# Optimization experiments

Measured on AMD Instinct MI355X. Metric: run time of the kernel, lower is better.

## Reference

```python
import jax, jax.numpy as jnp
import numpy as np

N_NODES = 50000   # total nodes across the batch of graphs
N_EDGES = 800000  # avg degree 16
F_IN = 128        # num_features
DIM = 256         # hidden dim
N_LAYERS = 3      # num_gc_layers
N_GRAPHS = 512    # graphs in the batch (max(batch)+1)
BN_EPS = 1e-5


def setup_inputs() -> dict:
    key = jax.random.key(0)
    ks = jax.random.split(key, 16)
    inp = {}
    inp["x"] = jax.random.normal(ks[0], (N_NODES, F_IN), dtype=jnp.float32)
    inp["edge_index"] = jax.random.randint(ks[1], (2, N_EDGES), 0, N_NODES, dtype=jnp.int64)
    inp["batch"] = jnp.sort(jax.random.randint(ks[2], (N_NODES,), 0, N_GRAPHS, dtype=jnp.int64))
    k = 3
    for i in range(N_LAYERS):
        fin = F_IN if i == 0 else DIM
        inp[f"w1_{i}"] = jax.random.normal(ks[k], (fin, DIM), dtype=jnp.float32) / np.sqrt(fin); k += 1
        inp[f"b1_{i}"] = jnp.zeros((DIM,), dtype=jnp.float32)
        inp[f"w2_{i}"] = jax.random.normal(ks[k], (DIM, DIM), dtype=jnp.float32) / np.sqrt(DIM); k += 1
        inp[f"b2_{i}"] = jnp.zeros((DIM,), dtype=jnp.float32)
        inp[f"bn_g{i}"] = jnp.ones((DIM,), dtype=jnp.float32)
        inp[f"bn_b{i}"] = jnp.zeros((DIM,), dtype=jnp.float32)
    return inp


def _gin_layer(h, src, dst, w1, b1, w2, b2, g, b):
    # GINConv (eps=0): agg_i = h_i + sum_{j->i} h_j  (scatter-add over edges)
    agg = h + jax.ops.segment_sum(h[src], dst, num_segments=N_NODES)
    # MLP: Linear -> ReLU -> Linear
    m = jnp.maximum(agg @ w1 + b1, 0.0) @ w2 + b2
    # F.relu then BatchNorm1d (training mode: batch statistics, biased var)
    m = jnp.maximum(m, 0.0)
    mu = m.mean(axis=0)
    var = ((m - mu) ** 2).mean(axis=0)
    return g * (m - mu) / jnp.sqrt(var + BN_EPS) + b


def reference(x, edge_index, batch,
              w1_0, b1_0, w2_0, b2_0, bn_g0, bn_b0,
              w1_1, b1_1, w2_1, b2_1, bn_g1, bn_b1,
              w1_2, b1_2, w2_2, b2_2, bn_g2, bn_b2):
    src, dst = edge_index[0], edge_index[1]
    params = [
        (w1_0, b1_0, w2_0, b2_0, bn_g0, bn_b0),
        (w1_1, b1_1, w2_1, b2_1, bn_g1, bn_b1),
        (w1_2, b1_2, w2_2, b2_2, bn_g2, bn_b2),
    ]
    xs = []
    h = x
    for p in params:
        h = _gin_layer(h, src, dst, *p)
        xs.append(h)
    # global add-pool readout per layer, concat along feature dim
    pooled = jnp.concatenate(
        [jax.ops.segment_sum(hi, batch, num_segments=N_GRAPHS) for hi in xs], axis=1)
    return pooled, jnp.concatenate(xs, axis=1)
```

## Files before the change

kernel.cpp:

```cpp
#include <hip/hip_runtime.h>

#define N_NODES 50000
#define N_EDGES 800000
#define F_IN 128
#define DIM 256
#define N_GRAPHS 512
#define BN_EPS 1e-5f

typedef unsigned short u16;
typedef unsigned int u32;
using floatx4 = __attribute__((ext_vector_type(4))) float;
using short8 = __attribute__((ext_vector_type(8))) short;

__device__ __forceinline__ u16 f2b(float f) {
    u32 u = __float_as_uint(f);
    return (u16)((u + 0x7fffu + ((u >> 16) & 1u)) >> 16);
}
__device__ __forceinline__ float blo(u32 u) { return __uint_as_float(u << 16); }
__device__ __forceinline__ float bhi(u32 u) { return __uint_as_float(u & 0xffff0000u); }
__device__ __forceinline__ u32 pack2(float a, float b) {
    return (u32)f2b(a) | ((u32)f2b(b) << 16);
}
__device__ __forceinline__ void load_lds16(const void* g, void* l) {
    __builtin_amdgcn_global_load_lds((const __attribute__((address_space(1))) void*)g,
                                     (__attribute__((address_space(3))) void*)l, 16, 0, 0);
}


__global__ void count_deg(const int* __restrict__ dst, int* __restrict__ deg, int nE) {
    int e = blockIdx.x * 256 + threadIdx.x;
    if (e < nE) atomicAdd(&deg[dst[e]], 1);
}

__global__ void scan_block(const int* __restrict__ deg, int* __restrict__ row_start,
                           int* __restrict__ bsum, int n) {
    __shared__ int wtot[4];
    int i = blockIdx.x * 256 + threadIdx.x;
    int lane = threadIdx.x & 63, w = threadIdx.x >> 6;
    int v = (i < n) ? deg[i] : 0;
    int s = v;
#pragma unroll
    for (int d = 1; d < 64; d <<= 1) {
        int t = __shfl_up(s, d);
        if (lane >= d) s += t;
    }
    if (lane == 63) wtot[w] = s;
    __syncthreads();
    int off = 0;
#pragma unroll
    for (int k = 0; k < 4; ++k)
        if (k < w) off += wtot[k];
    s += off;
    if (i < n) row_start[i + 1] = s;
    if (threadIdx.x == 255) bsum[blockIdx.x] = s;
}

__global__ void scan_partials(const int* __restrict__ bsum, int* __restrict__ boff,
                              int* __restrict__ row_start, int* __restrict__ cursor, int nb) {
    __shared__ int wtot[4];
    int i = threadIdx.x;
    int lane = i & 63, w = i >> 6;
    int v = (i < nb) ? bsum[i] : 0;
    int s = v;
#pragma unroll
    for (int d = 1; d < 64; d <<= 1) {
        int t = __shfl_up(s, d);
        if (lane >= d) s += t;
    }
    if (lane == 63) wtot[w] = s;
    __syncthreads();
    int off = 0;
#pragma unroll
    for (int k = 0; k < 4; ++k)
        if (k < w) off += wtot[k];
    boff[i] = s + off - v;
    if (i == 0) { row_start[0] = 0; cursor[0] = 0; }
}

__global__ void add_offsets(int* __restrict__ row_start, int* __restrict__ cursor,
                            const int* __restrict__ boff, int n) {
    int i = blockIdx.x * 256 + threadIdx.x;
    if (i < n) {
        int fin = row_start[i + 1] + boff[blockIdx.x];
        row_start[i + 1] = fin;
        cursor[i + 1] = fin;
    }
}

__global__ void fill_csr(const int* __restrict__ src, const int* __restrict__ dst,
                         int* __restrict__ cursor, int* __restrict__ srcs, int nE) {
    int e = blockIdx.x * 256 + threadIdx.x;
    if (e < nE) {
        int p = atomicAdd(&cursor[dst[e]], 1);
        srcs[p] = src[e];
    }
}


__global__ void convert_x4(const float4* __restrict__ in, uint2* __restrict__ out, int n4) {
    int i = blockIdx.x * 256 + threadIdx.x;
    if (i < n4) {
        float4 v = in[i];
        uint2 p;
        p.x = pack2(v.x, v.y);
        p.y = pack2(v.z, v.w);
        out[i] = p;
    }
}

__global__ void conv_wt(const float* __restrict__ w, u16* __restrict__ wt, int K) {
    int idx = blockIdx.x * 256 + threadIdx.x;
    if (idx >= 256 * K) return;
    int nn = idx / K, kk = idx - nn * K;
    wt[idx] = f2b(w[(size_t)kk * 256 + nn]);
}


template <int F>
__global__ void aggregate_bf16(const u16* __restrict__ h, const int* __restrict__ row_start,
                               const int* __restrict__ srcs, u16* __restrict__ outp, int n) {
    constexpr int NWD = F / 128;
    int node = (int)(((size_t)blockIdx.x * blockDim.x + threadIdx.x) >> 6);
    int lane = threadIdx.x & 63;
    if (node >= n) return;
    const u32* base = (const u32*)h;
    int cw = lane * NWD;
    float acc[2 * NWD];
#pragma unroll
    for (int t = 0; t < NWD; ++t) {
        u32 v0 = base[(size_t)node * (F / 2) + cw + t];
        acc[2 * t] = blo(v0);
        acc[2 * t + 1] = bhi(v0);
    }
    int s = row_start[node], e = row_start[node + 1];
    for (int j0 = s; j0 < e; j0 += 64) {
        int myidx = (j0 + lane < e) ? srcs[j0 + lane] : 0;
        int cnt = min(64, e - j0);
        int j = 0;
        for (; j + 3 < cnt; j += 4) {
            int s0 = __shfl(myidx, j);
            int s1 = __shfl(myidx, j + 1);
            int s2 = __shfl(myidx, j + 2);
            int s3 = __shfl(myidx, j + 3);
            u32 a0[NWD], a1[NWD], a2[NWD], a3[NWD];
#pragma unroll
            for (int t = 0; t < NWD; ++t) a0[t] = base[(size_t)s0 * (F / 2) + cw + t];
#pragma unroll
            for (int t = 0; t < NWD; ++t) a1[t] = base[(size_t)s1 * (F / 2) + cw + t];
#pragma unroll
            for (int t = 0; t < NWD; ++t) a2[t] = base[(size_t)s2 * (F / 2) + cw + t];
#pragma unroll
            for (int t = 0; t < NWD; ++t) a3[t] = base[(size_t)s3 * (F / 2) + cw + t];
#pragma unroll
            for (int t = 0; t < NWD; ++t) {
                acc[2 * t]     += (blo(a0[t]) + blo(a1[t])) + (blo(a2[t]) + blo(a3[t]));
                acc[2 * t + 1] += (bhi(a0[t]) + bhi(a1[t])) + (bhi(a2[t]) + bhi(a3[t]));
            }
        }
        for (; j < cnt; ++j) {
            int s0 = __shfl(myidx, j);
            u32 a0[NWD];
#pragma unroll
            for (int t = 0; t < NWD; ++t) a0[t] = base[(size_t)s0 * (F / 2) + cw + t];
#pragma unroll
            for (int t = 0; t < NWD; ++t) {
                acc[2 * t] += blo(a0[t]);
                acc[2 * t + 1] += bhi(a0[t]);
            }
        }
    }
    u32* op = (u32*)outp;
#pragma unroll
    for (int t = 0; t < NWD; ++t)
        op[(size_t)node * (F / 2) + cw + t] = pack2(acc[2 * t], acc[2 * t + 1]);
}


template <int MODE>
__global__ __launch_bounds__(256) void gemm_mfma(
    const u16* __restrict__ A, const u16* __restrict__ Bt, const float* __restrict__ bias,
    void* __restrict__ Cout, float* __restrict__ sums, int M, int K) {
    __shared__ u16 As[128 * 32];
    __shared__ u16 Bs[128 * 32];
    const int tid = threadIdx.x;
    const int w = tid >> 6, lane = tid & 63;
    const int wm = w >> 1, wn = w & 1;
    const int r = lane & 15, rg = lane >> 4;
    const int bm = blockIdx.x * 128;
    const int bn = blockIdx.y * 128;

    floatx4 acc[4][4];
#pragma unroll
    for (int i = 0; i < 4; ++i)
#pragma unroll
        for (int j = 0; j < 4; ++j) acc[i][j] = (floatx4){0.f, 0.f, 0.f, 0.f};

    for (int k0 = 0; k0 < K; k0 += 32) {
        __syncthreads();
#pragma unroll
        for (int q = 0; q < 2; ++q) {
            int i = q * 256 + tid;
            int ar = bm + (i >> 2);
            if (ar >= M) ar = M - 1;
            load_lds16(A + (size_t)ar * K + k0 + (i & 3) * 8, As + (q * 4 + w) * 512);
            int nr = bn + (i >> 2);
            load_lds16(Bt + (size_t)nr * K + k0 + (i & 3) * 8, Bs + (q * 4 + w) * 512);
        }
        __syncthreads();
        short8 a[4], b[4];
#pragma unroll
        for (int mi = 0; mi < 4; ++mi)
            a[mi] = *(const short8*)(As + (wm * 64 + mi * 16 + r) * 32 + rg * 8);
#pragma unroll
        for (int ni = 0; ni < 4; ++ni)
            b[ni] = *(const short8*)(Bs + (wn * 64 + ni * 16 + r) * 32 + rg * 8);
#pragma unroll
        for (int mi = 0; mi < 4; ++mi)
#pragma unroll
            for (int ni = 0; ni < 4; ++ni)
                acc[mi][ni] = __builtin_amdgcn_mfma_f32_16x16x32_bf16(a[mi], b[ni], acc[mi][ni], 0, 0, 0);
    }

    if (MODE == 0) {
        u16* C = (u16*)Cout;
#pragma unroll
        for (int ni = 0; ni < 4; ++ni) {
            int col = bn + wn * 64 + ni * 16 + r;
            float bv = bias[col];
#pragma unroll
            for (int mi = 0; mi < 4; ++mi)
#pragma unroll
                for (int rr = 0; rr < 4; ++rr) {
                    int row = bm + wm * 64 + mi * 16 + rg * 4 + rr;
                    if (row < M) C[(size_t)row * 256 + col] = f2b(fmaxf(acc[mi][ni][rr] + bv, 0.f));
                }
        }
    } else {
        float* C = (float*)Cout;
#pragma unroll
        for (int ni = 0; ni < 4; ++ni) {
            int col = bn + wn * 64 + ni * 16 + r;
            float bv = bias[col];
            float s = 0.f, s2 = 0.f;
#pragma unroll
            for (int mi = 0; mi < 4; ++mi)
#pragma unroll
                for (int rr = 0; rr < 4; ++rr) {
                    int row = bm + wm * 64 + mi * 16 + rg * 4 + rr;
                    if (row < M) {
                        float v = fmaxf(acc[mi][ni][rr] + bv, 0.f);
                        C[(size_t)row * 256 + col] = v;
                        s += v;
                        s2 += v * v;
                    }
                }
            s += __shfl_xor(s, 16);
            s += __shfl_xor(s, 32);
            s2 += __shfl_xor(s2, 16);
            s2 += __shfl_xor(s2, 32);
            if (rg == 0) {
                atomicAdd(&sums[col], s);
                atomicAdd(&sums[256 + col], s2);
            }
        }
    }
}


__global__ void bn_finalize(const float* __restrict__ sums, const float* __restrict__ g,
                            const float* __restrict__ b, float* __restrict__ ss, float inv_n) {
    int c = threadIdx.x;
    float mu = sums[c] * inv_n;
    float var = sums[256 + c] * inv_n - mu * mu;
    float sc = g[c] / sqrtf(var + BN_EPS);
    ss[c] = sc;
    ss[256 + c] = b[c] - mu * sc;
}


template <int WRITE_H>
__global__ void bn_apply_pool(const float* __restrict__ Mfp, const float* __restrict__ ss,
                              const int* __restrict__ batch, float* __restrict__ out_nodes,
                              u16* __restrict__ H, float* __restrict__ pooled,
                              int col_off, int n) {
    int w = threadIdx.x >> 6, lane = threadIdx.x & 63;
    int base = blockIdx.x * 64 + w * 16;
    if (base >= n) return;
    int c4 = lane << 2;
    float4 sc = *(const float4*)(ss + c4);
    float4 sh = *(const float4*)(ss + 256 + c4);
    float4 acc = make_float4(0.f, 0.f, 0.f, 0.f);
    int gcur = -1;
    int end = min(base + 16, n);
    for (int row = base; row < end; ++row) {
        float4 v = *(const float4*)(Mfp + (size_t)row * 256 + c4);
        float4 o;
        o.x = fmaf(v.x, sc.x, sh.x);
        o.y = fmaf(v.y, sc.y, sh.y);
        o.z = fmaf(v.z, sc.z, sh.z);
        o.w = fmaf(v.w, sc.w, sh.w);
        *(float4*)(out_nodes + (size_t)row * 768 + col_off + c4) = o;
        if (WRITE_H) {
            uint2 pk;
            pk.x = pack2(o.x, o.y);
            pk.y = pack2(o.z, o.w);
            *(uint2*)(H + (size_t)row * 256 + c4) = pk;
        }
        int g = batch[row];
        if (g != gcur) {
            if (gcur >= 0) {
                float* pp = pooled + (size_t)gcur * 768 + col_off + c4;
                atomicAdd(pp + 0, acc.x);
                atomicAdd(pp + 1, acc.y);
                atomicAdd(pp + 2, acc.z);
                atomicAdd(pp + 3, acc.w);
            }
            gcur = g;
            acc = o;
        } else {
            acc.x += o.x; acc.y += o.y; acc.z += o.z; acc.w += o.w;
        }
    }
    if (gcur >= 0) {
        float* pp = pooled + (size_t)gcur * 768 + col_off + c4;
        atomicAdd(pp + 0, acc.x);
        atomicAdd(pp + 1, acc.y);
        atomicAdd(pp + 2, acc.z);
        atomicAdd(pp + 3, acc.w);
    }
}


extern "C" void kernel_launch(void* const* d_in, const int* in_sizes, int n_in,
                              void* d_out, int out_size, void* d_ws, size_t ws_size,
                              hipStream_t stream) {
    const float* x = (const float*)d_in[0];
    const int* esrc = (const int*)d_in[1];
    const int* edst = esrc + N_EDGES;
    const int* batch = (const int*)d_in[2];

    const float* w1[3] = {(const float*)d_in[3], (const float*)d_in[9], (const float*)d_in[15]};
    const float* b1[3] = {(const float*)d_in[4], (const float*)d_in[10], (const float*)d_in[16]};
    const float* w2[3] = {(const float*)d_in[5], (const float*)d_in[11], (const float*)d_in[17]};
    const float* b2[3] = {(const float*)d_in[6], (const float*)d_in[12], (const float*)d_in[18]};
    const float* bng[3] = {(const float*)d_in[7], (const float*)d_in[13], (const float*)d_in[19]};
    const float* bnb[3] = {(const float*)d_in[8], (const float*)d_in[14], (const float*)d_in[20]};

    float* out_pooled = (float*)d_out;
    float* out_nodes = (float*)d_out + (size_t)N_GRAPHS * 768;

    char* p = (char*)d_ws;
    float* Mfp = (float*)p;
    u16* Abf = (u16*)p;
    p += (size_t)N_NODES * 256 * 4;
    u16* T = (u16*)p;  p += (size_t)N_NODES * 256 * 2;
    u16* H = (u16*)p;  p += (size_t)N_NODES * 256 * 2;
    u16* W1t[3]; u16* W2t[3];
    W1t[0] = (u16*)p; p += 256 * 128 * 2;
    W1t[1] = (u16*)p; p += 256 * 256 * 2;
    W1t[2] = (u16*)p; p += 256 * 256 * 2;
    for (int L = 0; L < 3; ++L) { W2t[L] = (u16*)p; p += 256 * 256 * 2; }
    float* sums = (float*)p; p += 512 * 4;
    float* ss = (float*)p;   p += 512 * 4;
    int* deg = (int*)p;       p += (size_t)N_NODES * 4;
    int* row_start = (int*)p; p += (size_t)(N_NODES + 1) * 4;
    int* cursor = (int*)p;    p += (size_t)(N_NODES + 1) * 4;
    int* srcs = (int*)p;      p += (size_t)N_EDGES * 4;
    int* bsum = (int*)p;      p += 256 * 4;
    int* boff = (int*)p;      p += 256 * 4;

    const int NBLK = (N_NODES + 255) / 256;

    hipMemsetAsync(deg, 0, N_NODES * sizeof(int), stream);
    count_deg<<<(N_EDGES + 255) / 256, 256, 0, stream>>>(edst, deg, N_EDGES);
    scan_block<<<NBLK, 256, 0, stream>>>(deg, row_start, bsum, N_NODES);
    scan_partials<<<1, 256, 0, stream>>>(bsum, boff, row_start, cursor, NBLK);
    add_offsets<<<NBLK, 256, 0, stream>>>(row_start, cursor, boff, N_NODES);
    fill_csr<<<(N_EDGES + 255) / 256, 256, 0, stream>>>(esrc, edst, cursor, srcs, N_EDGES);

    hipMemsetAsync(out_pooled, 0, (size_t)N_GRAPHS * 768 * sizeof(float), stream);
    convert_x4<<<(N_NODES * F_IN / 4 + 255) / 256, 256, 0, stream>>>(
        (const float4*)x, (uint2*)H, N_NODES * F_IN / 4);
    for (int L = 0; L < 3; ++L) {
        int K1 = (L == 0) ? F_IN : DIM;
        conv_wt<<<(256 * K1 + 255) / 256, 256, 0, stream>>>(w1[L], W1t[L], K1);
        conv_wt<<<(256 * 256 + 255) / 256, 256, 0, stream>>>(w2[L], W2t[L], 256);
    }

    dim3 ggrid((N_NODES + 127) / 128, 2);
    const int PBLK = (N_NODES + 63) / 64;
    for (int L = 0; L < 3; ++L) {
        int K1 = (L == 0) ? F_IN : DIM;
        if (L == 0)
            aggregate_bf16<128><<<(N_NODES + 3) / 4, 256, 0, stream>>>(H, row_start, srcs, Abf, N_NODES);
        else
            aggregate_bf16<256><<<(N_NODES + 3) / 4, 256, 0, stream>>>(H, row_start, srcs, Abf, N_NODES);
        gemm_mfma<0><<<ggrid, 256, 0, stream>>>(Abf, W1t[L], b1[L], (void*)T, nullptr, N_NODES, K1);
        hipMemsetAsync(sums, 0, 512 * sizeof(float), stream);
        gemm_mfma<1><<<ggrid, 256, 0, stream>>>(T, W2t[L], b2[L], (void*)Mfp, sums, N_NODES, DIM);
        bn_finalize<<<1, 256, 0, stream>>>(sums, bng[L], bnb[L], ss, 1.0f / N_NODES);
        if (L < 2)
            bn_apply_pool<1><<<PBLK, 256, 0, stream>>>(Mfp, ss, batch, out_nodes, H, out_pooled, L * 256, N_NODES);
        else
            bn_apply_pool<0><<<PBLK, 256, 0, stream>>>(Mfp, ss, batch, out_nodes, H, out_pooled, L * 256, N_NODES);
    }
}
```

Baseline: 803.6 us.

## Cut launches, widen GEMM tiles to full N, deepen gather unroll in aggregation

Weight and input conversions are merged into a single kernel, and all BN sum buffers are zeroed with one memset. bn_finalize is folded into bn_apply_pool, which removes several small launches per layer. The GEMM now runs 512 threads per block, each block covering all 256 output columns, so A tiles are loaded once instead of twice. The aggregation loop issues 8 gathers in flight instead of 4 to raise memory-level parallelism, at the cost of more registers.

```diff
diff --git a/kernel.cpp b/kernel.cpp
--- a/kernel.cpp
+++ b/kernel.cpp
@@ -97,22 +97,33 @@
 }
 
 
-__global__ void convert_x4(const float4* __restrict__ in, uint2* __restrict__ out, int n4) {
+__global__ void convert_all(const float4* __restrict__ x4, uint2* __restrict__ Hout, int n4,
+                            const float* __restrict__ w10, const float* __restrict__ w11,
+                            const float* __restrict__ w12, const float* __restrict__ w20,
+                            const float* __restrict__ w21, const float* __restrict__ w22,
+                            u16* __restrict__ Wall) {
     int i = blockIdx.x * 256 + threadIdx.x;
     if (i < n4) {
-        float4 v = in[i];
+        float4 v = x4[i];
         uint2 p;
         p.x = pack2(v.x, v.y);
         p.y = pack2(v.z, v.w);
-        out[i] = p;
-    }
-}
-
-__global__ void conv_wt(const float* __restrict__ w, u16* __restrict__ wt, int K) {
-    int idx = blockIdx.x * 256 + threadIdx.x;
-    if (idx >= 256 * K) return;
-    int nn = idx / K, kk = idx - nn * K;
-    wt[idx] = f2b(w[(size_t)kk * 256 + nn]);
+        Hout[i] = p;
+        return;
+    }
+    int j = i - n4;
+    if (j >= 360448) return;
+    const float* w;
+    int K, base;
+    if (j < 32768)       { w = w10; K = 128; base = 0; }
+    else if (j < 98304)  { w = w11; K = 256; base = 32768; }
+    else if (j < 163840) { w = w12; K = 256; base = 98304; }
+    else if (j < 229376) { w = w20; K = 256; base = 163840; }
+    else if (j < 294912) { w = w21; K = 256; base = 229376; }
+    else                 { w = w22; K = 256; base = 294912; }
+    int loc = j - base;
+    int nn = loc / K, kk = loc - nn * K;
+    Wall[j] = f2b(w[(size_t)kk * 256 + nn]);
 }
 
 
@@ -137,25 +148,37 @@
         int myidx = (j0 + lane < e) ? srcs[j0 + lane] : 0;
         int cnt = min(64, e - j0);
         int j = 0;
+        for (; j + 7 < cnt; j += 8) {
+            u32 a[8][NWD];
+#pragma unroll
+            for (int q = 0; q < 8; ++q) {
+                int sq = __shfl(myidx, j + q);
+#pragma unroll
+                for (int t = 0; t < NWD; ++t) a[q][t] = base[(size_t)sq * (F / 2) + cw + t];
+            }
+#pragma unroll
+            for (int q = 0; q < 8; ++q)
+#pragma unroll
+                for (int t = 0; t < NWD; ++t) {
+                    acc[2 * t] += blo(a[q][t]);
+                    acc[2 * t + 1] += bhi(a[q][t]);
+                }
+        }
         for (; j + 3 < cnt; j += 4) {
-            int s0 = __shfl(myidx, j);
-            int s1 = __shfl(myidx, j + 1);
-            int s2 = __shfl(myidx, j + 2);
-            int s3 = __shfl(myidx, j + 3);
-            u32 a0[NWD], a1[NWD], a2[NWD], a3[NWD];
-#pragma unroll
-            for (int t = 0; t < NWD; ++t) a0[t] = base[(size_t)s0 * (F / 2) + cw + t];
-#pragma unroll
-            for (int t = 0; t < NWD; ++t) a1[t] = base[(size_t)s1 * (F / 2) + cw + t];
-#pragma unroll
-            for (int t = 0; t < NWD; ++t) a2[t] = base[(size_t)s2 * (F / 2) + cw + t];
-#pragma unroll
-            for (int t = 0; t < NWD; ++t) a3[t] = base[(size_t)s3 * (F / 2) + cw + t];
-#pragma unroll
-            for (int t = 0; t < NWD; ++t) {
-                acc[2 * t]     += (blo(a0[t]) + blo(a1[t])) + (blo(a2[t]) + blo(a3[t]));
-                acc[2 * t + 1] += (bhi(a0[t]) + bhi(a1[t])) + (bhi(a2[t]) + bhi(a3[t]));
-            }
+            u32 a[4][NWD];
+#pragma unroll
+            for (int q = 0; q < 4; ++q) {
+                int sq = __shfl(myidx, j + q);
+#pragma unroll
+                for (int t = 0; t < NWD; ++t) a[q][t] = base[(size_t)sq * (F / 2) + cw + t];
+            }
+#pragma unroll
+            for (int q = 0; q < 4; ++q)
+#pragma unroll
+                for (int t = 0; t < NWD; ++t) {
+                    acc[2 * t] += blo(a[q][t]);
+                    acc[2 * t + 1] += bhi(a[q][t]);
+                }
         }
         for (; j < cnt; ++j) {
             int s0 = __shfl(myidx, j);
@@ -177,17 +200,16 @@
 
 
 template <int MODE>
-__global__ __launch_bounds__(256) void gemm_mfma(
+__global__ __launch_bounds__(512) void gemm_mfma(
     const u16* __restrict__ A, const u16* __restrict__ Bt, const float* __restrict__ bias,
     void* __restrict__ Cout, float* __restrict__ sums, int M, int K) {
     __shared__ u16 As[128 * 32];
-    __shared__ u16 Bs[128 * 32];
+    __shared__ u16 Bs[256 * 32];
     const int tid = threadIdx.x;
     const int w = tid >> 6, lane = tid & 63;
-    const int wm = w >> 1, wn = w & 1;
+    const int wm = w >> 2, wn = w & 3;
     const int r = lane & 15, rg = lane >> 4;
     const int bm = blockIdx.x * 128;
-    const int bn = blockIdx.y * 128;
 
     floatx4 acc[4][4];
 #pragma unroll
@@ -197,14 +219,16 @@
 
     for (int k0 = 0; k0 < K; k0 += 32) {
         __syncthreads();
-#pragma unroll
-        for (int q = 0; q < 2; ++q) {
-            int i = q * 256 + tid;
-            int ar = bm + (i >> 2);
-            if (ar >= M) ar = M - 1;
-            load_lds16(A + (size_t)ar * K + k0 + (i & 3) * 8, As + (q * 4 + w) * 512);
-            int nr = bn + (i >> 2);
-            load_lds16(Bt + (size_t)nr * K + k0 + (i & 3) * 8, Bs + (q * 4 + w) * 512);
+        {
+            int arow = bm + (tid >> 2);
+            if (arow >= M) arow = M - 1;
+            load_lds16(A + (size_t)arow * K + k0 + (tid & 3) * 8, As + w * 512);
+#pragma unroll
+            for (int q = 0; q < 2; ++q) {
+                int i = q * 512 + tid;
+                int nrow = i >> 2;
+                load_lds16(Bt + (size_t)nrow * K + k0 + (i & 3) * 8, Bs + (q * 8 + w) * 512);
+            }
         }
         __syncthreads();
         short8 a[4], b[4];
@@ -225,7 +249,7 @@
         u16* C = (u16*)Cout;
 #pragma unroll
         for (int ni = 0; ni < 4; ++ni) {
-            int col = bn + wn * 64 + ni * 16 + r;
+            int col = wn * 64 + ni * 16 + r;
             float bv = bias[col];
 #pragma unroll
             for (int mi = 0; mi < 4; ++mi)
@@ -239,7 +263,7 @@
         float* C = (float*)Cout;
 #pragma unroll
         for (int ni = 0; ni < 4; ++ni) {
-            int col = bn + wn * 64 + ni * 16 + r;
+            int col = wn * 64 + ni * 16 + r;
             float bv = bias[col];
             float s = 0.f, s2 = 0.f;
 #pragma unroll
@@ -267,28 +291,32 @@
 }
 
 
-__global__ void bn_finalize(const float* __restrict__ sums, const float* __restrict__ g,
-                            const float* __restrict__ b, float* __restrict__ ss, float inv_n) {
-    int c = threadIdx.x;
-    float mu = sums[c] * inv_n;
-    float var = sums[256 + c] * inv_n - mu * mu;
-    float sc = g[c] / sqrtf(var + BN_EPS);
-    ss[c] = sc;
-    ss[256 + c] = b[c] - mu * sc;
-}
-
-
 template <int WRITE_H>
-__global__ void bn_apply_pool(const float* __restrict__ Mfp, const float* __restrict__ ss,
+__global__ void bn_apply_pool(const float* __restrict__ Mfp, const float* __restrict__ sums,
+                              const float* __restrict__ g, const float* __restrict__ bb,
                               const int* __restrict__ batch, float* __restrict__ out_nodes,
                               u16* __restrict__ H, float* __restrict__ pooled,
-                              int col_off, int n) {
+                              int col_off, int n, float inv_n) {
     int w = threadIdx.x >> 6, lane = threadIdx.x & 63;
     int base = blockIdx.x * 64 + w * 16;
     if (base >= n) return;
     int c4 = lane << 2;
-    float4 sc = *(const float4*)(ss + c4);
-    float4 sh = *(const float4*)(ss + 256 + c4);
+    float4 s1 = *(const float4*)(sums + c4);
+    float4 s2 = *(const float4*)(sums + 256 + c4);
+    float4 g4 = *(const float4*)(g + c4);
+    float4 b4 = *(const float4*)(bb + c4);
+    float4 sc, sh;
+    {
+        float mux = s1.x * inv_n, muy = s1.y * inv_n, muz = s1.z * inv_n, muw = s1.w * inv_n;
+        sc.x = g4.x / sqrtf(s2.x * inv_n - mux * mux + BN_EPS);
+        sc.y = g4.y / sqrtf(s2.y * inv_n - muy * muy + BN_EPS);
+        sc.z = g4.z / sqrtf(s2.z * inv_n - muz * muz + BN_EPS);
+        sc.w = g4.w / sqrtf(s2.w * inv_n - muw * muw + BN_EPS);
+        sh.x = b4.x - mux * sc.x;
+        sh.y = b4.y - muy * sc.y;
+        sh.z = b4.z - muz * sc.z;
+        sh.w = b4.w - muw * sc.w;
+    }
     float4 acc = make_float4(0.f, 0.f, 0.f, 0.f);
     int gcur = -1;
     int end = min(base + 16, n);
@@ -306,8 +334,8 @@
             pk.y = pack2(o.z, o.w);
             *(uint2*)(H + (size_t)row * 256 + c4) = pk;
         }
-        int g = batch[row];
-        if (g != gcur) {
+        int gg = batch[row];
+        if (gg != gcur) {
             if (gcur >= 0) {
                 float* pp = pooled + (size_t)gcur * 768 + col_off + c4;
                 atomicAdd(pp + 0, acc.x);
@@ -315,7 +343,7 @@
                 atomicAdd(pp + 2, acc.z);
                 atomicAdd(pp + 3, acc.w);
             }
-            gcur = g;
+            gcur = gg;
             acc = o;
         } else {
             acc.x += o.x; acc.y += o.y; acc.z += o.z; acc.w += o.w;
@@ -355,53 +383,54 @@
     p += (size_t)N_NODES * 256 * 4;
     u16* T = (u16*)p;  p += (size_t)N_NODES * 256 * 2;
     u16* H = (u16*)p;  p += (size_t)N_NODES * 256 * 2;
-    u16* W1t[3]; u16* W2t[3];
-    W1t[0] = (u16*)p; p += 256 * 128 * 2;
-    W1t[1] = (u16*)p; p += 256 * 256 * 2;
-    W1t[2] = (u16*)p; p += 256 * 256 * 2;
-    for (int L = 0; L < 3; ++L) { W2t[L] = (u16*)p; p += 256 * 256 * 2; }
-    float* sums = (float*)p; p += 512 * 4;
-    float* ss = (float*)p;   p += 512 * 4;
-    int* deg = (int*)p;       p += (size_t)N_NODES * 4;
+    u16* Wall = (u16*)p; p += (size_t)360448 * 2;
+    float* sums = (float*)p; p += 3 * 512 * 4;
+    int* deg = (int*)p;      p += (size_t)N_NODES * 4;
+    const size_t zero_bytes = 3 * 512 * 4 + (size_t)N_NODES * 4;
     int* row_start = (int*)p; p += (size_t)(N_NODES + 1) * 4;
     int* cursor = (int*)p;    p += (size_t)(N_NODES + 1) * 4;
     int* srcs = (int*)p;      p += (size_t)N_EDGES * 4;
     int* bsum = (int*)p;      p += 256 * 4;
     int* boff = (int*)p;      p += 256 * 4;
 
+    const u16* W1t[3] = {Wall, Wall + 32768, Wall + 98304};
+    const u16* W2t[3] = {Wall + 163840, Wall + 229376, Wall + 294912};
+
     const int NBLK = (N_NODES + 255) / 256;
 
-    hipMemsetAsync(deg, 0, N_NODES * sizeof(int), stream);
+    hipMemsetAsync(sums, 0, zero_bytes, stream);
+    hipMemsetAsync(out_pooled, 0, (size_t)N_GRAPHS * 768 * sizeof(float), stream);
+
     count_deg<<<(N_EDGES + 255) / 256, 256, 0, stream>>>(edst, deg, N_EDGES);
     scan_block<<<NBLK, 256, 0, stream>>>(deg, row_start, bsum, N_NODES);
     scan_partials<<<1, 256, 0, stream>>>(bsum, boff, row_start, cursor, NBLK);
     add_offsets<<<NBLK, 256, 0, stream>>>(row_start, cursor, boff, N_NODES);
     fill_csr<<<(N_EDGES + 255) / 256, 256, 0, stream>>>(esrc, edst, cursor, srcs, N_EDGES);
 
-    hipMemsetAsync(out_pooled, 0, (size_t)N_GRAPHS * 768 * sizeof(float), stream);
-    convert_x4<<<(N_NODES * F_IN / 4 + 255) / 256, 256, 0, stream>>>(
-        (const float4*)x, (uint2*)H, N_NODES * F_IN / 4);
-    for (int L = 0; L < 3; ++L) {
-        int K1 = (L == 0) ? F_IN : DIM;
-        conv_wt<<<(256 * K1 + 255) / 256, 256, 0, stream>>>(w1[L], W1t[L], K1);
-        conv_wt<<<(256 * 256 + 255) / 256, 256, 0, stream>>>(w2[L], W2t[L], 256);
-    }
-
-    dim3 ggrid((N_NODES + 127) / 128, 2);
+    {
+        const int n4 = N_NODES * F_IN / 4;
+        const int tot = n4 + 360448;
+        convert_all<<<(tot + 255) / 256, 256, 0, stream>>>(
+            (const float4*)x, (uint2*)H, n4,
+            w1[0], w1[1], w1[2], w2[0], w2[1], w2[2], Wall);
+    }
+
+    const int GGRID = (N_NODES + 127) / 128;
     const int PBLK = (N_NODES + 63) / 64;
     for (int L = 0; L < 3; ++L) {
         int K1 = (L == 0) ? F_IN : DIM;
+        float* sumsL = sums + L * 512;
         if (L == 0)
             aggregate_bf16<128><<<(N_NODES + 3) / 4, 256, 0, stream>>>(H, row_start, srcs, Abf, N_NODES);
         else
             aggregate_bf16<256><<<(N_NODES + 3) / 4, 256, 0, stream>>>(H, row_start, srcs, Abf, N_NODES);
-        gemm_mfma<0><<<ggrid, 256, 0, stream>>>(Abf, W1t[L], b1[L], (void*)T, nullptr, N_NODES, K1);
-        hipMemsetAsync(sums, 0, 512 * sizeof(float), stream);
-        gemm_mfma<1><<<ggrid, 256, 0, stream>>>(T, W2t[L], b2[L], (void*)Mfp, sums, N_NODES, DIM);
-        bn_finalize<<<1, 256, 0, stream>>>(sums, bng[L], bnb[L], ss, 1.0f / N_NODES);
+        gemm_mfma<0><<<GGRID, 512, 0, stream>>>(Abf, W1t[L], b1[L], (void*)T, nullptr, N_NODES, K1);
+        gemm_mfma<1><<<GGRID, 512, 0, stream>>>(T, W2t[L], b2[L], (void*)Mfp, sumsL, N_NODES, DIM);
         if (L < 2)
-            bn_apply_pool<1><<<PBLK, 256, 0, stream>>>(Mfp, ss, batch, out_nodes, H, out_pooled, L * 256, N_NODES);
+            bn_apply_pool<1><<<PBLK, 256, 0, stream>>>(Mfp, sumsL, bng[L], bnb[L], batch,
+                                                       out_nodes, H, out_pooled, L * 256, N_NODES, 1.0f / N_NODES);
         else
-            bn_apply_pool<0><<<PBLK, 256, 0, stream>>>(Mfp, ss, batch, out_nodes, H, out_pooled, L * 256, N_NODES);
-    }
-}
+            bn_apply_pool<0><<<PBLK, 256, 0, stream>>>(Mfp, sumsL, bng[L], bnb[L], batch,
+                                                       out_nodes, H, out_pooled, L * 256, N_NODES, 1.0f / N_NODES);
+    }
+}
```

After: 723.2 us. -10.0%, faster.
